# Optimization experiments

Hardware: AMD Instinct MI355X
Metric: run time of the kernel (lower is better)

## Reference

```python
import jax, jax.numpy as jnp
import numpy as np

N_TOKENS = 8192
IN_FEATURES = 4096
OUT_FEATURES = 4096


def setup_inputs() -> dict:
    key = jax.random.key(0)
    kx, kw, ks = jax.random.split(key, 3)
    x = jax.random.normal(kx, (N_TOKENS, IN_FEATURES), dtype=jnp.float32)
    # int8 weight in [-127, 126], per torch.randint(-127, 127, ...)
    weight = jax.random.randint(kw, (OUT_FEATURES, IN_FEATURES), -127, 127, dtype=jnp.int32).astype(jnp.int8)
    weight_scales = jax.random.uniform(ks, (OUT_FEATURES,), dtype=jnp.float32, minval=0.001, maxval=0.01)
    bias = jnp.zeros((1, OUT_FEATURES), dtype=jnp.float32)
    return {"x": x, "weight": weight, "weight_scales": weight_scales, "bias": bias}


def reference(x, weight, weight_scales, bias):
    # --- dynamic per-token activation quantization (min-max / abs-max) ---
    # scale per token so that max |x| maps to 127
    x_absmax = jnp.max(jnp.abs(x), axis=-1, keepdims=True)          # [T, 1]
    x_scale = x_absmax / 127.0                                       # [T, 1]
    q_x = jnp.clip(jnp.round(x / x_scale), -127, 127).astype(jnp.int8)  # [T, K]

    # --- int8 GEMM with int32 accumulation: q_y = q_x @ weight.T ---
    q_y = jax.lax.dot_general(
        q_x, weight,
        dimension_numbers=(((1,), (1,)), ((), ())),
        preferred_element_type=jnp.int32,
    )                                                                # [T, N] int32

    # --- dequantize: per-channel weight scale x per-token activation scale ---
    y = q_y.astype(jnp.float32) * weight_scales[None, :] * x_scale   # [T, N]
    y = y + bias
    return y
```

## Files before the change

kernel.cpp:

```cpp
#include <hip/hip_runtime.h>
#include <cstdint>
#include <cstddef>

#define T_TOKENS 8192
#define K_DIM 4096
#define N_DIM 4096

using i32x4 = __attribute__((ext_vector_type(4))) int;

__global__ __launch_bounds__(256) void pack_weight(const int* __restrict__ win,
                                                   int8_t* __restrict__ wout) {
    const int idx = blockIdx.x * 256 + threadIdx.x;
    const i32x4 v = reinterpret_cast<const i32x4*>(win)[idx];
    uint32_t pk = (uint32_t)(v.x & 255) | ((uint32_t)(v.y & 255) << 8) |
                  ((uint32_t)(v.z & 255) << 16) | ((uint32_t)(v.w & 255) << 24);
    reinterpret_cast<int*>(wout)[idx] = (int)pk;
}

__global__ __launch_bounds__(256) void quant_rows(const float* __restrict__ x,
                                                  int8_t* __restrict__ qx,
                                                  float* __restrict__ xscale) {
    const int t = blockIdx.x;
    const int tid = threadIdx.x;
    const float4* row = reinterpret_cast<const float4*>(x + (size_t)t * K_DIM);

    float4 v[4];
    float amax = 0.0f;
#pragma unroll
    for (int i = 0; i < 4; ++i) {
        v[i] = row[i * 256 + tid];
        amax = fmaxf(amax, fabsf(v[i].x));
        amax = fmaxf(amax, fabsf(v[i].y));
        amax = fmaxf(amax, fabsf(v[i].z));
        amax = fmaxf(amax, fabsf(v[i].w));
    }
#pragma unroll
    for (int off = 32; off > 0; off >>= 1)
        amax = fmaxf(amax, __shfl_xor(amax, off));

    __shared__ float red[4];
    if ((tid & 63) == 0) red[tid >> 6] = amax;
    __syncthreads();
    amax = fmaxf(fmaxf(red[0], red[1]), fmaxf(red[2], red[3]));

    const float scale = fmaxf(amax, 1e-30f) * (1.0f / 127.0f);
    if (tid == 0) xscale[t] = scale;

    int* qrow = reinterpret_cast<int*>(qx + (size_t)t * K_DIM);
#pragma unroll
    for (int i = 0; i < 4; ++i) {
        int q0 = (int)fminf(fmaxf(rintf(v[i].x / scale), -127.0f), 127.0f);
        int q1 = (int)fminf(fmaxf(rintf(v[i].y / scale), -127.0f), 127.0f);
        int q2 = (int)fminf(fmaxf(rintf(v[i].z / scale), -127.0f), 127.0f);
        int q3 = (int)fminf(fmaxf(rintf(v[i].w / scale), -127.0f), 127.0f);
        uint32_t pk = (uint32_t)(q0 & 255) | ((uint32_t)(q1 & 255) << 8) |
                      ((uint32_t)(q2 & 255) << 16) | ((uint32_t)(q3 & 255) << 24);
        qrow[i * 256 + tid] = (int)pk;
    }
}

__global__ __launch_bounds__(256) void int8_gemm(const int8_t* __restrict__ qx,
                                                 const int8_t* __restrict__ w,
                                                 const float* __restrict__ xscale,
                                                 const float* __restrict__ wscale,
                                                 const float* __restrict__ bias,
                                                 float* __restrict__ out) {
    __shared__ int8_t As[128 * 64];
    __shared__ int8_t Bs[128 * 64];

    const int tid = threadIdx.x;
    const int lane = tid & 63;
    const int wave = tid >> 6;
    const int wr = wave >> 1;
    const int wc = wave & 1;
    const int l16 = lane & 15;
    const int quad = lane >> 4;

    const size_t a_row0 = (size_t)blockIdx.x * 128;
    const size_t b_row0 = (size_t)blockIdx.y * 128;

    const int s_row = tid >> 2;
    const int s_col = (tid & 3) * 16;

    const int8_t* ag0 = qx + (a_row0 + s_row) * (size_t)K_DIM + s_col;
    const int8_t* ag1 = ag0 + (size_t)64 * K_DIM;
    const int8_t* bg0 = w + (b_row0 + s_row) * (size_t)K_DIM + s_col;
    const int8_t* bg1 = bg0 + (size_t)64 * K_DIM;

    i32x4* As4 = reinterpret_cast<i32x4*>(As);
    i32x4* Bs4 = reinterpret_cast<i32x4*>(Bs);

    i32x4 acc[4][4] = {};

    i32x4 ra0 = *reinterpret_cast<const i32x4*>(ag0);
    i32x4 ra1 = *reinterpret_cast<const i32x4*>(ag1);
    i32x4 rb0 = *reinterpret_cast<const i32x4*>(bg0);
    i32x4 rb1 = *reinterpret_cast<const i32x4*>(bg1);

    for (int k0 = 0; k0 < K_DIM; k0 += 64) {
        __syncthreads();
        As4[tid] = ra0;
        As4[tid + 256] = ra1;
        Bs4[tid] = rb0;
        Bs4[tid + 256] = rb1;
        __syncthreads();

        const int k1 = k0 + 64;
        if (k1 < K_DIM) {
            ra0 = *reinterpret_cast<const i32x4*>(ag0 + k1);
            ra1 = *reinterpret_cast<const i32x4*>(ag1 + k1);
            rb0 = *reinterpret_cast<const i32x4*>(bg0 + k1);
            rb1 = *reinterpret_cast<const i32x4*>(bg1 + k1);
        }

        i32x4 af[4], bf[4];
#pragma unroll
        for (int i = 0; i < 4; ++i) {
            af[i] = As4[((wr * 64 + i * 16 + l16) * 64 + quad * 16) >> 4];
            bf[i] = Bs4[((wc * 64 + i * 16 + l16) * 64 + quad * 16) >> 4];
        }
#pragma unroll
        for (int i = 0; i < 4; ++i)
#pragma unroll
            for (int j = 0; j < 4; ++j)
                acc[i][j] = __builtin_amdgcn_mfma_i32_16x16x64_i8(af[i], bf[j], acc[i][j], 0, 0, 0);
    }

#pragma unroll
    for (int j = 0; j < 4; ++j) {
        const int n = (int)b_row0 + wc * 64 + j * 16 + l16;
        const float ws = wscale[n];
        const float bs = bias[n];
#pragma unroll
        for (int i = 0; i < 4; ++i) {
#pragma unroll
            for (int r = 0; r < 4; ++r) {
                const int t = (int)a_row0 + wr * 64 + i * 16 + quad * 4 + r;
                const float xs = xscale[t];
                out[(size_t)t * N_DIM + n] = (float)acc[i][j][r] * ws * xs + bs;
            }
        }
    }
}

extern "C" void kernel_launch(void* const* d_in, const int* in_sizes, int n_in,
                              void* d_out, int out_size, void* d_ws, size_t ws_size,
                              hipStream_t stream) {
    const float* x = (const float*)d_in[0];
    const int* w_i32 = (const int*)d_in[1];
    const float* wscale = (const float*)d_in[2];
    const float* bias = (const float*)d_in[3];
    float* out = (float*)d_out;

    int8_t* qx = (int8_t*)d_ws;
    float* xscale = (float*)((char*)d_ws + (size_t)T_TOKENS * K_DIM);
    int8_t* wpk = (int8_t*)((char*)d_ws + (size_t)T_TOKENS * K_DIM + 65536);

    pack_weight<<<(N_DIM * K_DIM / 4) / 256, 256, 0, stream>>>(w_i32, wpk);

    quant_rows<<<T_TOKENS, 256, 0, stream>>>(x, qx, xscale);

    dim3 grid(T_TOKENS / 128, N_DIM / 128);
    int8_gemm<<<grid, 256, 0, stream>>>(qx, wpk, xscale, wscale, bias, out);
}
```

Measured before the change: 474.8 us.

## Rewrite int8 GEMM with 256x256 tiles, direct-to-LDS loads and double buffering

```diff
diff --git a/kernel.cpp b/kernel.cpp
--- a/kernel.cpp
+++ b/kernel.cpp
@@ -5,6 +5,7 @@
 #define T_TOKENS 8192
 #define K_DIM 4096
 #define N_DIM 4096
+#define K_TILES 32
 
 using i32x4 = __attribute__((ext_vector_type(4))) int;
 
@@ -59,88 +60,155 @@
     }
 }
 
-__global__ __launch_bounds__(256) void int8_gemm(const int8_t* __restrict__ qx,
-                                                 const int8_t* __restrict__ w,
-                                                 const float* __restrict__ xscale,
-                                                 const float* __restrict__ wscale,
-                                                 const float* __restrict__ bias,
-                                                 float* __restrict__ out) {
-    __shared__ int8_t As[128 * 64];
-    __shared__ int8_t Bs[128 * 64];
+__global__ __launch_bounds__(512, 2) void int8_gemm(const int8_t* __restrict__ qx,
+                                                    const int8_t* __restrict__ w,
+                                                    const float* __restrict__ xscale,
+                                                    const float* __restrict__ wscale,
+                                                    const float* __restrict__ bias,
+                                                    float* __restrict__ out) {
+    extern __shared__ int8_t lds[];
 
     const int tid = threadIdx.x;
     const int lane = tid & 63;
     const int wave = tid >> 6;
-    const int wr = wave >> 1;
-    const int wc = wave & 1;
+    const int wr = wave >> 2;
+    const int wn = wave & 3;
     const int l16 = lane & 15;
     const int quad = lane >> 4;
 
-    const size_t a_row0 = (size_t)blockIdx.x * 128;
-    const size_t b_row0 = (size_t)blockIdx.y * 128;
+    const int wg = ((blockIdx.x & 7) << 6) | ((int)blockIdx.x >> 3);
+    const int tm = wg >> 4;
+    const int tn = wg & 15;
+
+    const int8_t* gA = qx + (size_t)tm * 256 * K_DIM;
+    const int8_t* gB = w + (size_t)tn * 256 * K_DIM;
 
     const int s_row = tid >> 2;
-    const int s_col = (tid & 3) * 16;
-
-    const int8_t* ag0 = qx + (a_row0 + s_row) * (size_t)K_DIM + s_col;
-    const int8_t* ag1 = ag0 + (size_t)64 * K_DIM;
-    const int8_t* bg0 = w + (b_row0 + s_row) * (size_t)K_DIM + s_col;
-    const int8_t* bg1 = bg0 + (size_t)64 * K_DIM;
-
-    i32x4* As4 = reinterpret_cast<i32x4*>(As);
-    i32x4* Bs4 = reinterpret_cast<i32x4*>(Bs);
-
-    i32x4 acc[4][4] = {};
-
-    i32x4 ra0 = *reinterpret_cast<const i32x4*>(ag0);
-    i32x4 ra1 = *reinterpret_cast<const i32x4*>(ag1);
-    i32x4 rb0 = *reinterpret_cast<const i32x4*>(bg0);
-    i32x4 rb1 = *reinterpret_cast<const i32x4*>(bg1);
-
-    for (int k0 = 0; k0 < K_DIM; k0 += 64) {
-        __syncthreads();
-        As4[tid] = ra0;
-        As4[tid + 256] = ra1;
-        Bs4[tid] = rb0;
-        Bs4[tid + 256] = rb1;
-        __syncthreads();
-
-        const int k1 = k0 + 64;
-        if (k1 < K_DIM) {
-            ra0 = *reinterpret_cast<const i32x4*>(ag0 + k1);
-            ra1 = *reinterpret_cast<const i32x4*>(ag1 + k1);
-            rb0 = *reinterpret_cast<const i32x4*>(bg0 + k1);
-            rb1 = *reinterpret_cast<const i32x4*>(bg1 + k1);
+    const int scol = (((tid & 3) ^ ((tid >> 3) & 3)) << 4);
+    const int fcol = ((quad ^ ((l16 >> 1) & 3)) << 4);
+
+    const int ldsA_rd = (wr * 128 + l16) * 64 + fcol;
+    const int ldsB_rd = 32768 + (wn * 64 + l16) * 64 + fcol;
+
+#define STAGE2(buf, op, ksl, k0)                                                        \
+    {                                                                                   \
+        const int8_t* g_ = ((op) ? gB : gA) +                                           \
+                           ((size_t)s_row * K_DIM + (size_t)((k0) + (ksl) * 64 + scol));\
+        int8_t* l_ = lds + (buf) * 65536 + (op) * 32768 + (ksl) * 16384 + tid * 16;     \
+        __builtin_amdgcn_global_load_lds(                                               \
+            (const __attribute__((address_space(1))) void*)g_,                          \
+            (__attribute__((address_space(3))) void*)l_, 16, 0, 0);                     \
+        __builtin_amdgcn_global_load_lds(                                               \
+            (const __attribute__((address_space(1))) void*)(g_ + (size_t)128 * K_DIM),  \
+            (__attribute__((address_space(3))) void*)(l_ + 8192), 16, 0, 0);            \
+    }
+
+    i32x4 acc[8][4] = {};
+    i32x4 af[4], bf[4];
+
+#define READ_B(buf, ksl)                                                     \
+    {                                                                        \
+        const int8_t* sB_ = lds + (buf) * 65536 + (ksl) * 16384 + ldsB_rd;   \
+        _Pragma("unroll") for (int nj = 0; nj < 4; ++nj)                     \
+            bf[nj] = *(const i32x4*)(sB_ + nj * 1024);                       \
+    }
+#define READ_A(buf, ksl, mh)                                                 \
+    {                                                                        \
+        const int8_t* sA_ =                                                  \
+            lds + (buf) * 65536 + (ksl) * 16384 + (mh) * 4096 + ldsA_rd;     \
+        _Pragma("unroll") for (int q = 0; q < 4; ++q)                        \
+            af[q] = *(const i32x4*)(sA_ + q * 1024);                         \
+    }
+#define MFMA16(mh)                                                           \
+    __builtin_amdgcn_s_setprio(1);                                           \
+    _Pragma("unroll") for (int q = 0; q < 4; ++q) {                          \
+        _Pragma("unroll") for (int nj = 0; nj < 4; ++nj)                     \
+            acc[(mh) * 4 + q][nj] = __builtin_amdgcn_mfma_i32_16x16x64_i8(   \
+                af[q], bf[nj], acc[(mh) * 4 + q][nj], 0, 0, 0);              \
+    }                                                                        \
+    __builtin_amdgcn_s_setprio(0);
+
+    STAGE2(0, 0, 0, 0)
+    STAGE2(0, 1, 0, 0)
+    STAGE2(0, 0, 1, 0)
+    STAGE2(0, 1, 1, 0)
+
+    for (int t = 0; t < K_TILES - 1; ++t) {
+        const int cur = t & 1;
+        const int nxt = cur ^ 1;
+        const int k1 = (t + 1) << 7;
+
+        STAGE2(nxt, 0, 0, k1)
+        asm volatile("s_waitcnt vmcnt(6)" ::: "memory");
+        __builtin_amdgcn_s_barrier();
+        READ_B(cur, 0)
+        READ_A(cur, 0, 0)
+        MFMA16(0)
+        __builtin_amdgcn_s_barrier();
+
+        STAGE2(nxt, 1, 0, k1)
+        READ_A(cur, 0, 1)
+        MFMA16(1)
+        __builtin_amdgcn_s_barrier();
+
+        STAGE2(nxt, 0, 1, k1)
+        asm volatile("s_waitcnt vmcnt(6)" ::: "memory");
+        __builtin_amdgcn_s_barrier();
+        READ_B(cur, 1)
+        READ_A(cur, 1, 0)
+        MFMA16(0)
+        __builtin_amdgcn_s_barrier();
+
+        STAGE2(nxt, 1, 1, k1)
+        READ_A(cur, 1, 1)
+        MFMA16(1)
+        __builtin_amdgcn_s_barrier();
+    }
+
+    {
+        asm volatile("s_waitcnt vmcnt(4)" ::: "memory");
+        __builtin_amdgcn_s_barrier();
+        READ_B(1, 0)
+        READ_A(1, 0, 0)
+        MFMA16(0)
+        __builtin_amdgcn_s_barrier();
+        READ_A(1, 0, 1)
+        MFMA16(1)
+        __builtin_amdgcn_s_barrier();
+        asm volatile("s_waitcnt vmcnt(0)" ::: "memory");
+        __builtin_amdgcn_s_barrier();
+        READ_B(1, 1)
+        READ_A(1, 1, 0)
+        MFMA16(0)
+        __builtin_amdgcn_s_barrier();
+        READ_A(1, 1, 1)
+        MFMA16(1)
+    }
+
+    const int row_base = tm * 256 + wr * 128 + quad * 4;
+    const int col_base = tn * 256 + wn * 64 + l16;
+    float wsv[4], bsv[4];
+#pragma unroll
+    for (int nj = 0; nj < 4; ++nj) {
+        wsv[nj] = wscale[col_base + nj * 16];
+        bsv[nj] = bias[col_base + nj * 16];
+    }
+#pragma unroll
+    for (int mi = 0; mi < 8; ++mi) {
+#pragma unroll
+        for (int r = 0; r < 4; ++r) {
+            const int trow = row_base + mi * 16 + r;
+            const float xs = xscale[trow];
+            float* orow = out + (size_t)trow * N_DIM + col_base;
+#pragma unroll
+            for (int nj = 0; nj < 4; ++nj)
+                orow[nj * 16] = (float)acc[mi][nj][r] * (wsv[nj] * xs) + bsv[nj];
         }
-
-        i32x4 af[4], bf[4];
-#pragma unroll
-        for (int i = 0; i < 4; ++i) {
-            af[i] = As4[((wr * 64 + i * 16 + l16) * 64 + quad * 16) >> 4];
-            bf[i] = Bs4[((wc * 64 + i * 16 + l16) * 64 + quad * 16) >> 4];
-        }
-#pragma unroll
-        for (int i = 0; i < 4; ++i)
-#pragma unroll
-            for (int j = 0; j < 4; ++j)
-                acc[i][j] = __builtin_amdgcn_mfma_i32_16x16x64_i8(af[i], bf[j], acc[i][j], 0, 0, 0);
-    }
-
-#pragma unroll
-    for (int j = 0; j < 4; ++j) {
-        const int n = (int)b_row0 + wc * 64 + j * 16 + l16;
-        const float ws = wscale[n];
-        const float bs = bias[n];
-#pragma unroll
-        for (int i = 0; i < 4; ++i) {
-#pragma unroll
-            for (int r = 0; r < 4; ++r) {
-                const int t = (int)a_row0 + wr * 64 + i * 16 + quad * 4 + r;
-                const float xs = xscale[t];
-                out[(size_t)t * N_DIM + n] = (float)acc[i][j][r] * ws * xs + bs;
-            }
-        }
-    }
+    }
+#undef STAGE2
+#undef READ_B
+#undef READ_A
+#undef MFMA16
 }
 
 extern "C" void kernel_launch(void* const* d_in, const int* in_sizes, int n_in,
@@ -156,10 +224,14 @@
     float* xscale = (float*)((char*)d_ws + (size_t)T_TOKENS * K_DIM);
     int8_t* wpk = (int8_t*)((char*)d_ws + (size_t)T_TOKENS * K_DIM + 65536);
 
+    static bool attr_set = false;
+    if (!attr_set) {
+        (void)hipFuncSetAttribute(reinterpret_cast<const void*>(&int8_gemm),
+                                  hipFuncAttributeMaxDynamicSharedMemorySize, 131072);
+        attr_set = true;
+    }
+
     pack_weight<<<(N_DIM * K_DIM / 4) / 256, 256, 0, stream>>>(w_i32, wpk);
-
     quant_rows<<<T_TOKENS, 256, 0, stream>>>(x, qx, xscale);
-
-    dim3 grid(T_TOKENS / 128, N_DIM / 128);
-    int8_gemm<<<grid, 256, 0, stream>>>(qx, wpk, xscale, wscale, bias, out);
-}
+    int8_gemm<<<dim3(512), dim3(512), 131072, stream>>>(qx, wpk, xscale, wscale, bias, out);
+}
```

After: 389.4 us. 1.22x faster.
